# Performance work log

Hardware: AMD Instinct MI355X
Metric: run time of the kernel (lower is better)

The kernel has to match this reference:

```python
import jax, jax.numpy as jnp
import numpy as np

B = 8       # number of point clouds
N = 4096    # points per cloud (start_point)
M = 1024    # sampled points per cloud (sampled_point_ammount), ratio 0.25
D = 64      # feature dim


def setup_inputs() -> dict:
    key = jax.random.key(0)
    k1, k2 = jax.random.split(key)
    x = jax.random.normal(k1, (B * N, D), dtype=jnp.float32)
    pos = jax.random.uniform(k2, (B * N, 3), dtype=jnp.float32)
    batch = jnp.repeat(jnp.arange(B, dtype=jnp.int32), N)  # sorted batch ids
    return {"x": x, "pos": pos, "batch": batch}


def _fps_single(pos_b, m):
    # Farthest point sampling on one cloud [N,3]; deterministic start at index 0.
    n = pos_b.shape[0]
    big = jnp.asarray(jnp.finfo(pos_b.dtype).max, pos_b.dtype)

    def step(carry, _):
        mind, last = carry
        d = jnp.sum((pos_b - pos_b[last]) ** 2, axis=-1)  # [N]
        mind = jnp.minimum(mind, d)
        nxt = jnp.argmax(mind).astype(jnp.int32)
        return (mind, nxt), nxt

    init = (jnp.full((n,), big, pos_b.dtype), jnp.int32(0))
    _, rest = jax.lax.scan(step, init, None, length=m - 1)
    return jnp.concatenate([jnp.zeros((1,), jnp.int32), rest])  # [M]


def reference(x, pos, batch):
    pos_b = pos.reshape(B, N, 3)
    # --- DownsampleMRG: FPS gather (scale_factor = M/N) ---
    idx = jax.vmap(lambda p: _fps_single(p, M))(pos_b)              # [B, M] local idx
    gidx = (idx + jnp.arange(B, dtype=jnp.int32)[:, None] * N).reshape(-1)
    x_lr = x[gidx]                                                  # [B*M, D]
    pos_lr = pos[gidx]                                              # [B*M, 3]
    # --- UpsampleMRG: lr_x = cat([x_lr, pos_lr]); knn_interpolate k=1 ---
    lr_feat = jnp.concatenate([x_lr, pos_lr], axis=1).reshape(B, M, D + 3)
    pos_lr_b = pos_lr.reshape(B, M, 3)
    # pairwise squared distances hr->lr within each cloud: [B, N, M]
    d2 = jnp.sum((pos_b[:, :, None, :] - pos_lr_b[:, None, :, :]) ** 2, axis=-1)
    nn = jnp.argmin(d2, axis=-1)                                    # [B, N]
    # k=1 interpolation: weights normalize to 1 -> pure nearest-neighbor gather
    interp = jnp.take_along_axis(lr_feat, nn[:, :, None], axis=1).reshape(B * N, D + 3)
    # out_x = cat([x_hr, pos_hr, interpolated lr features])
    out_x = jnp.concatenate([x, pos, interp], axis=1)               # [B*N, D+3+D+3]
    return out_x, jnp.zeros((out_x.shape[0], 3), pos.dtype), batch
```

## Files before the change

### kernel.cpp

```cpp
#include <hip/hip_runtime.h>
#include <cstdint>

#define BATCH 8
#define NPTS  4096
#define MPTS  1024
#define DIM   64

typedef float v2f __attribute__((ext_vector_type(2)));
typedef unsigned long long u64;
typedef unsigned int u32;

__device__ __forceinline__ double mk_key(float m, u32 aux) {
  const u64 k = ((u64)__float_as_uint(m) << 32) | (u64)aux;
  return __longlong_as_double((long long)k);
}
__device__ __forceinline__ u32 key_lo(double d) {
  return (u32)(u64)__double_as_longlong(d);
}

#define WAVE_MAX_F64_STEP(x, ctrl)                                                    \
  {                                                                                   \
    const u64 xu_ = (u64)__double_as_longlong(x);                                     \
    const int lo_ = __builtin_amdgcn_update_dpp(0, (int)(u32)xu_, (ctrl), 0xf, 0xf, true);  \
    const int hi_ = __builtin_amdgcn_update_dpp(0, (int)(u32)(xu_ >> 32), (ctrl), 0xf, 0xf, true); \
    const double y_ = __longlong_as_double((long long)(((u64)(u32)hi_ << 32) | (u64)(u32)lo_)); \
    (x) = fmax((x), y_);                                                              \
  }

__global__ __launch_bounds__(256) void fps_kernel(const float* __restrict__ pos,
                                                  int* __restrict__ gidx) {
#pragma clang fp contract(off)
  const int b = blockIdx.x;
  const int t = threadIdx.x;
  const float* p = pos + (size_t)b * NPTS * 3;

  __shared__ float4 sp[NPTS];
  __shared__ double red[2][4];

  v2f px[8], py[8], pz[8], mind[8];
#pragma unroll
  for (int k = 0; k < 16; ++k) {
    const int i = t + k * 256;
    const float a = p[3 * i + 0];
    const float c = p[3 * i + 1];
    const float d = p[3 * i + 2];
    sp[i] = make_float4(a, c, d, 0.0f);
    px[k >> 1][k & 1] = a;
    py[k >> 1][k & 1] = c;
    pz[k >> 1][k & 1] = d;
    mind[k >> 1][k & 1] = 3.402823466e+38f;
  }
  __syncthreads();

  if (t == 0) gidx[b * MPTS] = b * NPTS;
  float4 w = sp[0];
  float lx = w.x, ly = w.y, lz = w.z;

  for (int it = 1; it < MPTS; ++it) {
    const v2f vlx = {lx, lx}, vly = {ly, ly}, vlz = {lz, lz};
    double pg[8];
#pragma unroll
    for (int g = 0; g < 8; ++g) {
      const v2f dx = px[g] - vlx;
      const v2f dy = py[g] - vly;
      const v2f dz = pz[g] - vlz;
      const v2f d = (dx * dx + dy * dy) + dz * dz;
      const v2f m = __builtin_elementwise_min(mind[g], d);
      mind[g] = m;
      const double p0 = mk_key(m[0], ~(u32)(t + (2 * g) * 256));
      const double p1 = mk_key(m[1], ~(u32)(t + (2 * g + 1) * 256));
      pg[g] = fmax(p0, p1);
    }
    const double b0 = fmax(pg[0], pg[1]);
    const double b1 = fmax(pg[2], pg[3]);
    const double b2 = fmax(pg[4], pg[5]);
    const double b3 = fmax(pg[6], pg[7]);
    double best = fmax(fmax(b0, b1), fmax(b2, b3));

    WAVE_MAX_F64_STEP(best, 0x111);
    WAVE_MAX_F64_STEP(best, 0x112);
    WAVE_MAX_F64_STEP(best, 0x114);
    WAVE_MAX_F64_STEP(best, 0x118);
    WAVE_MAX_F64_STEP(best, 0x142);
    WAVE_MAX_F64_STEP(best, 0x143);

    const int buf = it & 1;
    if ((t & 63) == 63) red[buf][t >> 6] = best;
    __syncthreads();

    const double c = fmax(fmax(red[buf][0], red[buf][1]),
                          fmax(red[buf][2], red[buf][3]));
    const u32 widx = ~key_lo(c);

    w = sp[widx];
    lx = w.x; ly = w.y; lz = w.z;
    if (t == 0) gidx[b * MPTS + it] = b * NPTS + (int)widx;
  }
}

__global__ __launch_bounds__(256) void nn_kernel(const float* __restrict__ pos,
                                                 const int* __restrict__ gidx,
                                                 int* __restrict__ nng) {
#pragma clang fp contract(off)
  const int b = blockIdx.x >> 5;
  const int chunk = blockIdx.x & 31;
  const int t = threadIdx.x;

  __shared__ float lrx[MPTS], lry[MPTS], lrz[MPTS];
  for (int j = t; j < MPTS; j += 256) {
    const int g = gidx[b * MPTS + j];
    lrx[j] = pos[3 * g + 0];
    lry[j] = pos[3 * g + 1];
    lrz[j] = pos[3 * g + 2];
  }
  __syncthreads();

  const int pt = chunk * 128 + (t >> 1);
  const int half = t & 1;
  const int i = b * NPTS + pt;
  const float x = pos[3 * i + 0];
  const float y = pos[3 * i + 1];
  const float z = pos[3 * i + 2];
  const v2f vx = {x, x}, vy = {y, y}, vz = {z, z};

  double best = __longlong_as_double(0x7FEFFFFFFFFFFFFFll);
  const int j0 = half * 512;
#pragma unroll 4
  for (int s = 0; s < 256; ++s) {
    const int j = j0 + 2 * s;
    const v2f qx = *(const v2f*)&lrx[j];
    const v2f qy = *(const v2f*)&lry[j];
    const v2f qz = *(const v2f*)&lrz[j];
    const v2f dx = vx - qx;
    const v2f dy = vy - qy;
    const v2f dz = vz - qz;
    const v2f d = (dx * dx + dy * dy) + dz * dz;
    const double p0 = mk_key(d[0], (u32)j);
    const double p1 = mk_key(d[1], (u32)(j + 1));
    best = fmin(best, fmin(p0, p1));
  }
  const u64 bu = (u64)__double_as_longlong(best);
  const u64 ou = ((u64)(u32)__shfl_xor((int)(bu >> 32), 1, 64) << 32) |
                 (u64)(u32)__shfl_xor((int)(u32)bu, 1, 64);
  best = fmin(best, __longlong_as_double((long long)ou));
  if (half == 0) nng[i] = gidx[b * MPTS + (int)key_lo(best)];
}

__global__ __launch_bounds__(256) void assemble_kernel(const float* __restrict__ x,
                                                       const float* __restrict__ pos,
                                                       const int* __restrict__ batch,
                                                       const int* __restrict__ nng,
                                                       float* __restrict__ out) {
  const int w = (int)((blockIdx.x * 256 + threadIdx.x) >> 6);
  const int lane = threadIdx.x & 63;
  if (w >= BATCH * NPTS) return;
  const int g = nng[w];

  float* o = out + (size_t)w * 134;
  o[lane] = x[(size_t)w * DIM + lane];
  o[67 + lane] = x[(size_t)g * DIM + lane];
  if (lane < 3) {
    o[64 + lane] = pos[3 * w + lane];
    o[131 + lane] = pos[3 * g + lane];
  }

  float* o2 = out + (size_t)BATCH * NPTS * 134;
  if (lane < 3) o2[3 * w + lane] = 0.0f;
  float* o3 = o2 + (size_t)BATCH * NPTS * 3;
  if (lane == 0) o3[w] = (float)batch[w];
}

extern "C" void kernel_launch(void* const* d_in, const int* in_sizes, int n_in,
                              void* d_out, int out_size, void* d_ws, size_t ws_size,
                              hipStream_t stream) {
  const float* x = (const float*)d_in[0];
  const float* pos = (const float*)d_in[1];
  const int* batch = (const int*)d_in[2];

  int* gidx = (int*)d_ws;
  int* nng = gidx + BATCH * MPTS;

  float* out = (float*)d_out;

  fps_kernel<<<BATCH, 256, 0, stream>>>(pos, gidx);
  nn_kernel<<<BATCH * 32, 256, 0, stream>>>(pos, gidx, nng);
  assemble_kernel<<<(BATCH * NPTS * 64) / 256, 256, 0, stream>>>(x, pos, batch, nng, out);
}
```

Baseline: 575.8 us.

## Process two clouds per FPS block and fuse nearest-neighbor with output assembly

The FPS kernel now processes two point clouds per block, interleaving their independent distance/argmax chains so they share one barrier per iteration and expose more instruction-level parallelism. The shared-memory position copy is dropped and the selected point is re-read from global memory. The nearest-neighbor and assembly kernels are fused so neighbor indices stay in shared memory and one launch and round-trip are removed. This doubles register pressure in FPS and puts a global load on the serial critical path.

```diff
diff --git a/kernel.cpp b/kernel.cpp
--- a/kernel.cpp
+++ b/kernel.cpp
@@ -11,102 +11,136 @@
 typedef unsigned int u32;
 
 __device__ __forceinline__ double mk_key(float m, u32 aux) {
-  const u64 k = ((u64)__float_as_uint(m) << 32) | (u64)aux;
-  return __longlong_as_double((long long)k);
+  return __hiloint2double((int)__float_as_uint(m), (int)aux);
 }
 __device__ __forceinline__ u32 key_lo(double d) {
-  return (u32)(u64)__double_as_longlong(d);
-}
-
-#define WAVE_MAX_F64_STEP(x, ctrl)                                                    \
-  {                                                                                   \
-    const u64 xu_ = (u64)__double_as_longlong(x);                                     \
-    const int lo_ = __builtin_amdgcn_update_dpp(0, (int)(u32)xu_, (ctrl), 0xf, 0xf, true);  \
-    const int hi_ = __builtin_amdgcn_update_dpp(0, (int)(u32)(xu_ >> 32), (ctrl), 0xf, 0xf, true); \
-    const double y_ = __longlong_as_double((long long)(((u64)(u32)hi_ << 32) | (u64)(u32)lo_)); \
-    (x) = fmax((x), y_);                                                              \
-  }
-
-__global__ __launch_bounds__(256) void fps_kernel(const float* __restrict__ pos,
-                                                  int* __restrict__ gidx) {
+  return (u32)__double2loint(d);
+}
+
+#define WAVE_MAX_F64_STEP(x, ctrl)                                                   \
+  {                                                                                  \
+    const int lo_ = __builtin_amdgcn_update_dpp(0, __double2loint(x), (ctrl), 0xf, 0xf, true); \
+    const int hi_ = __builtin_amdgcn_update_dpp(0, __double2hiint(x), (ctrl), 0xf, 0xf, true); \
+    const double y_ = __hiloint2double(hi_, lo_);                                    \
+    (x) = fmax((x), y_);                                                             \
+  }
+
+__global__ __launch_bounds__(256, 1) void fps_kernel(const float* __restrict__ pos,
+                                                     int* __restrict__ gidx) {
 #pragma clang fp contract(off)
-  const int b = blockIdx.x;
+  const int b0 = blockIdx.x * 2, b1 = b0 + 1;
   const int t = threadIdx.x;
-  const float* p = pos + (size_t)b * NPTS * 3;
-
-  __shared__ float4 sp[NPTS];
-  __shared__ double red[2][4];
-
-  v2f px[8], py[8], pz[8], mind[8];
+  const float* pA = pos + (size_t)b0 * NPTS * 3;
+  const float* pB = pos + (size_t)b1 * NPTS * 3;
+
+  __shared__ double redA[2][4], redB[2][4];
+
+  v2f ax[8], ay[8], az[8], am[8];
+  v2f bx[8], by[8], bz[8], bm[8];
+  u32 aux[16];
 #pragma unroll
   for (int k = 0; k < 16; ++k) {
     const int i = t + k * 256;
-    const float a = p[3 * i + 0];
-    const float c = p[3 * i + 1];
-    const float d = p[3 * i + 2];
-    sp[i] = make_float4(a, c, d, 0.0f);
-    px[k >> 1][k & 1] = a;
-    py[k >> 1][k & 1] = c;
-    pz[k >> 1][k & 1] = d;
-    mind[k >> 1][k & 1] = 3.402823466e+38f;
-  }
-  __syncthreads();
-
-  if (t == 0) gidx[b * MPTS] = b * NPTS;
-  float4 w = sp[0];
-  float lx = w.x, ly = w.y, lz = w.z;
+    aux[k] = ~(u32)i;
+    ax[k >> 1][k & 1] = pA[3 * i + 0];
+    ay[k >> 1][k & 1] = pA[3 * i + 1];
+    az[k >> 1][k & 1] = pA[3 * i + 2];
+    bx[k >> 1][k & 1] = pB[3 * i + 0];
+    by[k >> 1][k & 1] = pB[3 * i + 1];
+    bz[k >> 1][k & 1] = pB[3 * i + 2];
+    am[k >> 1][k & 1] = 3.402823466e+38f;
+    bm[k >> 1][k & 1] = 3.402823466e+38f;
+  }
+
+  if (t == 0) {
+    gidx[b0 * MPTS] = b0 * NPTS;
+    gidx[b1 * MPTS] = b1 * NPTS;
+  }
+  float lxA = pA[0], lyA = pA[1], lzA = pA[2];
+  float lxB = pB[0], lyB = pB[1], lzB = pB[2];
 
   for (int it = 1; it < MPTS; ++it) {
-    const v2f vlx = {lx, lx}, vly = {ly, ly}, vlz = {lz, lz};
-    double pg[8];
-#pragma unroll
-    for (int g = 0; g < 8; ++g) {
-      const v2f dx = px[g] - vlx;
-      const v2f dy = py[g] - vly;
-      const v2f dz = pz[g] - vlz;
-      const v2f d = (dx * dx + dy * dy) + dz * dz;
-      const v2f m = __builtin_elementwise_min(mind[g], d);
-      mind[g] = m;
-      const double p0 = mk_key(m[0], ~(u32)(t + (2 * g) * 256));
-      const double p1 = mk_key(m[1], ~(u32)(t + (2 * g + 1) * 256));
-      pg[g] = fmax(p0, p1);
-    }
-    const double b0 = fmax(pg[0], pg[1]);
-    const double b1 = fmax(pg[2], pg[3]);
-    const double b2 = fmax(pg[4], pg[5]);
-    const double b3 = fmax(pg[6], pg[7]);
-    double best = fmax(fmax(b0, b1), fmax(b2, b3));
-
-    WAVE_MAX_F64_STEP(best, 0x111);
-    WAVE_MAX_F64_STEP(best, 0x112);
-    WAVE_MAX_F64_STEP(best, 0x114);
-    WAVE_MAX_F64_STEP(best, 0x118);
-    WAVE_MAX_F64_STEP(best, 0x142);
-    WAVE_MAX_F64_STEP(best, 0x143);
-
     const int buf = it & 1;
-    if ((t & 63) == 63) red[buf][t >> 6] = best;
+    double bestA;
+    {
+      const v2f vx = {lxA, lxA}, vy = {lyA, lyA}, vz = {lzA, lzA};
+      double pg[8];
+#pragma unroll
+      for (int g = 0; g < 8; ++g) {
+        const v2f dx = ax[g] - vx;
+        const v2f dy = ay[g] - vy;
+        const v2f dz = az[g] - vz;
+        const v2f d = (dx * dx + dy * dy) + dz * dz;
+        const v2f m = __builtin_elementwise_min(am[g], d);
+        am[g] = m;
+        pg[g] = fmax(mk_key(m[0], aux[2 * g]), mk_key(m[1], aux[2 * g + 1]));
+      }
+      bestA = fmax(fmax(fmax(pg[0], pg[1]), fmax(pg[2], pg[3])),
+                   fmax(fmax(pg[4], pg[5]), fmax(pg[6], pg[7])));
+      WAVE_MAX_F64_STEP(bestA, 0x111);
+      WAVE_MAX_F64_STEP(bestA, 0x112);
+      WAVE_MAX_F64_STEP(bestA, 0x114);
+      WAVE_MAX_F64_STEP(bestA, 0x118);
+      WAVE_MAX_F64_STEP(bestA, 0x142);
+      WAVE_MAX_F64_STEP(bestA, 0x143);
+    }
+    double bestB;
+    {
+      const v2f vx = {lxB, lxB}, vy = {lyB, lyB}, vz = {lzB, lzB};
+      double pg[8];
+#pragma unroll
+      for (int g = 0; g < 8; ++g) {
+        const v2f dx = bx[g] - vx;
+        const v2f dy = by[g] - vy;
+        const v2f dz = bz[g] - vz;
+        const v2f d = (dx * dx + dy * dy) + dz * dz;
+        const v2f m = __builtin_elementwise_min(bm[g], d);
+        bm[g] = m;
+        pg[g] = fmax(mk_key(m[0], aux[2 * g]), mk_key(m[1], aux[2 * g + 1]));
+      }
+      bestB = fmax(fmax(fmax(pg[0], pg[1]), fmax(pg[2], pg[3])),
+                   fmax(fmax(pg[4], pg[5]), fmax(pg[6], pg[7])));
+      WAVE_MAX_F64_STEP(bestB, 0x111);
+      WAVE_MAX_F64_STEP(bestB, 0x112);
+      WAVE_MAX_F64_STEP(bestB, 0x114);
+      WAVE_MAX_F64_STEP(bestB, 0x118);
+      WAVE_MAX_F64_STEP(bestB, 0x142);
+      WAVE_MAX_F64_STEP(bestB, 0x143);
+    }
+
+    if ((t & 63) == 63) {
+      redA[buf][t >> 6] = bestA;
+      redB[buf][t >> 6] = bestB;
+    }
     __syncthreads();
 
-    const double c = fmax(fmax(red[buf][0], red[buf][1]),
-                          fmax(red[buf][2], red[buf][3]));
-    const u32 widx = ~key_lo(c);
-
-    w = sp[widx];
-    lx = w.x; ly = w.y; lz = w.z;
-    if (t == 0) gidx[b * MPTS + it] = b * NPTS + (int)widx;
-  }
-}
-
-__global__ __launch_bounds__(256) void nn_kernel(const float* __restrict__ pos,
-                                                 const int* __restrict__ gidx,
-                                                 int* __restrict__ nng) {
+    const double cA = fmax(fmax(redA[buf][0], redA[buf][1]),
+                           fmax(redA[buf][2], redA[buf][3]));
+    const double cB = fmax(fmax(redB[buf][0], redB[buf][1]),
+                           fmax(redB[buf][2], redB[buf][3]));
+    const u32 wA = ~key_lo(cA);
+    const u32 wB = ~key_lo(cB);
+    const float3 qa = *(const float3*)(pA + 3 * (size_t)wA);
+    const float3 qb = *(const float3*)(pB + 3 * (size_t)wB);
+    lxA = qa.x; lyA = qa.y; lzA = qa.z;
+    lxB = qb.x; lyB = qb.y; lzB = qb.z;
+    if (t == 0) {
+      gidx[b0 * MPTS + it] = b0 * NPTS + (int)wA;
+      gidx[b1 * MPTS + it] = b1 * NPTS + (int)wB;
+    }
+  }
+}
+
+__global__ __launch_bounds__(256) void nn_assemble_kernel(
+    const float* __restrict__ x, const float* __restrict__ pos,
+    const int* __restrict__ gidx, float* __restrict__ out) {
 #pragma clang fp contract(off)
   const int b = blockIdx.x >> 5;
   const int chunk = blockIdx.x & 31;
   const int t = threadIdx.x;
 
   __shared__ float lrx[MPTS], lry[MPTS], lrz[MPTS];
+  __shared__ int snng[128];
   for (int j = t; j < MPTS; j += 256) {
     const int g = gidx[b * MPTS + j];
     lrx[j] = pos[3 * g + 0];
@@ -115,59 +149,53 @@
   }
   __syncthreads();
 
-  const int pt = chunk * 128 + (t >> 1);
-  const int half = t & 1;
-  const int i = b * NPTS + pt;
-  const float x = pos[3 * i + 0];
-  const float y = pos[3 * i + 1];
-  const float z = pos[3 * i + 2];
-  const v2f vx = {x, x}, vy = {y, y}, vz = {z, z};
-
-  double best = __longlong_as_double(0x7FEFFFFFFFFFFFFFll);
-  const int j0 = half * 512;
+  {
+    const int pt = chunk * 128 + (t >> 1);
+    const int half = t & 1;
+    const int i = b * NPTS + pt;
+    const float px = pos[3 * i + 0];
+    const float py = pos[3 * i + 1];
+    const float pz = pos[3 * i + 2];
+    const v2f vx = {px, px}, vy = {py, py}, vz = {pz, pz};
+
+    double best = __hiloint2double(0x7FEFFFFF, 0xFFFFFFFF);
+    const int j0 = half * 512;
 #pragma unroll 4
-  for (int s = 0; s < 256; ++s) {
-    const int j = j0 + 2 * s;
-    const v2f qx = *(const v2f*)&lrx[j];
-    const v2f qy = *(const v2f*)&lry[j];
-    const v2f qz = *(const v2f*)&lrz[j];
-    const v2f dx = vx - qx;
-    const v2f dy = vy - qy;
-    const v2f dz = vz - qz;
-    const v2f d = (dx * dx + dy * dy) + dz * dz;
-    const double p0 = mk_key(d[0], (u32)j);
-    const double p1 = mk_key(d[1], (u32)(j + 1));
-    best = fmin(best, fmin(p0, p1));
-  }
-  const u64 bu = (u64)__double_as_longlong(best);
-  const u64 ou = ((u64)(u32)__shfl_xor((int)(bu >> 32), 1, 64) << 32) |
-                 (u64)(u32)__shfl_xor((int)(u32)bu, 1, 64);
-  best = fmin(best, __longlong_as_double((long long)ou));
-  if (half == 0) nng[i] = gidx[b * MPTS + (int)key_lo(best)];
-}
-
-__global__ __launch_bounds__(256) void assemble_kernel(const float* __restrict__ x,
-                                                       const float* __restrict__ pos,
-                                                       const int* __restrict__ batch,
-                                                       const int* __restrict__ nng,
-                                                       float* __restrict__ out) {
-  const int w = (int)((blockIdx.x * 256 + threadIdx.x) >> 6);
-  const int lane = threadIdx.x & 63;
-  if (w >= BATCH * NPTS) return;
-  const int g = nng[w];
-
-  float* o = out + (size_t)w * 134;
-  o[lane] = x[(size_t)w * DIM + lane];
-  o[67 + lane] = x[(size_t)g * DIM + lane];
-  if (lane < 3) {
-    o[64 + lane] = pos[3 * w + lane];
-    o[131 + lane] = pos[3 * g + lane];
-  }
-
+    for (int s = 0; s < 256; ++s) {
+      const int j = j0 + 2 * s;
+      const v2f qx = *(const v2f*)&lrx[j];
+      const v2f qy = *(const v2f*)&lry[j];
+      const v2f qz = *(const v2f*)&lrz[j];
+      const v2f dx = vx - qx;
+      const v2f dy = vy - qy;
+      const v2f dz = vz - qz;
+      const v2f d = (dx * dx + dy * dy) + dz * dz;
+      best = fmin(best, fmin(mk_key(d[0], (u32)j), mk_key(d[1], (u32)(j + 1))));
+    }
+    const int blo = __shfl_xor(__double2loint(best), 1, 64);
+    const int bhi = __shfl_xor(__double2hiint(best), 1, 64);
+    best = fmin(best, __hiloint2double(bhi, blo));
+    if (half == 0) snng[t >> 1] = gidx[b * MPTS + (int)key_lo(best)];
+  }
+  __syncthreads();
+
+  const int wave = t >> 6, lane = t & 63;
   float* o2 = out + (size_t)BATCH * NPTS * 134;
-  if (lane < 3) o2[3 * w + lane] = 0.0f;
   float* o3 = o2 + (size_t)BATCH * NPTS * 3;
-  if (lane == 0) o3[w] = (float)batch[w];
+#pragma unroll
+  for (int r = wave; r < 128; r += 4) {
+    const int i = b * NPTS + chunk * 128 + r;
+    const int g = snng[r];
+    float* o = out + (size_t)i * 134;
+    o[lane] = x[(size_t)i * DIM + lane];
+    o[67 + lane] = x[(size_t)g * DIM + lane];
+    if (lane < 3) {
+      o[64 + lane] = pos[3 * i + lane];
+      o[131 + lane] = pos[3 * g + lane];
+      o2[3 * i + lane] = 0.0f;
+    }
+    if (lane == 0) o3[i] = (float)b;
+  }
 }
 
 extern "C" void kernel_launch(void* const* d_in, const int* in_sizes, int n_in,
@@ -175,14 +203,10 @@
                               hipStream_t stream) {
   const float* x = (const float*)d_in[0];
   const float* pos = (const float*)d_in[1];
-  const int* batch = (const int*)d_in[2];
 
   int* gidx = (int*)d_ws;
-  int* nng = gidx + BATCH * MPTS;
-
   float* out = (float*)d_out;
 
-  fps_kernel<<<BATCH, 256, 0, stream>>>(pos, gidx);
-  nn_kernel<<<BATCH * 32, 256, 0, stream>>>(pos, gidx, nng);
-  assemble_kernel<<<(BATCH * NPTS * 64) / 256, 256, 0, stream>>>(x, pos, batch, nng, out);
-}
+  fps_kernel<<<BATCH / 2, 256, 0, stream>>>(pos, gidx);
+  nn_assemble_kernel<<<BATCH * 32, 256, 0, stream>>>(x, pos, gidx, out);
+}
```

New measurement: 987.8 us. 71.6% more time.

## Widen FPS block to 512 threads and fuse NN search with output assembly

Applied to the files above, without the earlier changes.

The FPS kernel now runs 512 threads per cloud, so each thread holds 8 points instead of 16. Shared positions move from an array of float4 to separate x/y/z arrays, index keys are precomputed, and the cross-wave reduction grows to 8 waves. The nearest-neighbour and assembly kernels are merged: neighbour indices stay in shared memory and the same block writes the output rows, which removes one launch and the nng round-trip. The batch output is written as the block's cloud id instead of being read from the batch input, which relies on the batch ids being sorted and contiguous. The wider FPS block adds barrier and reduction cost on a loop that runs serially, one iteration per sample.

```diff
diff --git a/kernel.cpp b/kernel.cpp
--- a/kernel.cpp
+++ b/kernel.cpp
@@ -11,40 +11,40 @@
 typedef unsigned int u32;
 
 __device__ __forceinline__ double mk_key(float m, u32 aux) {
-  const u64 k = ((u64)__float_as_uint(m) << 32) | (u64)aux;
-  return __longlong_as_double((long long)k);
+  return __hiloint2double((int)__float_as_uint(m), (int)aux);
 }
 __device__ __forceinline__ u32 key_lo(double d) {
-  return (u32)(u64)__double_as_longlong(d);
+  return (u32)__double2loint(d);
 }
 
-#define WAVE_MAX_F64_STEP(x, ctrl)                                                    \
-  {                                                                                   \
-    const u64 xu_ = (u64)__double_as_longlong(x);                                     \
-    const int lo_ = __builtin_amdgcn_update_dpp(0, (int)(u32)xu_, (ctrl), 0xf, 0xf, true);  \
-    const int hi_ = __builtin_amdgcn_update_dpp(0, (int)(u32)(xu_ >> 32), (ctrl), 0xf, 0xf, true); \
-    const double y_ = __longlong_as_double((long long)(((u64)(u32)hi_ << 32) | (u64)(u32)lo_)); \
-    (x) = fmax((x), y_);                                                              \
+#define WAVE_MAX_F64_STEP(x, ctrl)                                                   \
+  {                                                                                  \
+    const int lo_ = __builtin_amdgcn_update_dpp(0, __double2loint(x), (ctrl), 0xf, 0xf, true); \
+    const int hi_ = __builtin_amdgcn_update_dpp(0, __double2hiint(x), (ctrl), 0xf, 0xf, true); \
+    const double y_ = __hiloint2double(hi_, lo_);                                    \
+    (x) = fmax((x), y_);                                                             \
   }
 
-__global__ __launch_bounds__(256) void fps_kernel(const float* __restrict__ pos,
+__global__ __launch_bounds__(512) void fps_kernel(const float* __restrict__ pos,
                                                   int* __restrict__ gidx) {
 #pragma clang fp contract(off)
   const int b = blockIdx.x;
   const int t = threadIdx.x;
   const float* p = pos + (size_t)b * NPTS * 3;
 
-  __shared__ float4 sp[NPTS];
-  __shared__ double red[2][4];
+  __shared__ float sx[NPTS], sy[NPTS], sz[NPTS];
+  __shared__ double red[2][8];
 
-  v2f px[8], py[8], pz[8], mind[8];
+  v2f px[4], py[4], pz[4], mind[4];
+  u32 aux[8];
 #pragma unroll
-  for (int k = 0; k < 16; ++k) {
-    const int i = t + k * 256;
+  for (int k = 0; k < 8; ++k) {
+    const int i = t + k * 512;
+    aux[k] = ~(u32)i;
     const float a = p[3 * i + 0];
     const float c = p[3 * i + 1];
     const float d = p[3 * i + 2];
-    sp[i] = make_float4(a, c, d, 0.0f);
+    sx[i] = a; sy[i] = c; sz[i] = d;
     px[k >> 1][k & 1] = a;
     py[k >> 1][k & 1] = c;
     pz[k >> 1][k & 1] = d;
@@ -53,29 +53,22 @@
   __syncthreads();
 
   if (t == 0) gidx[b * MPTS] = b * NPTS;
-  float4 w = sp[0];
-  float lx = w.x, ly = w.y, lz = w.z;
+  float lx = sx[0], ly = sy[0], lz = sz[0];
 
   for (int it = 1; it < MPTS; ++it) {
     const v2f vlx = {lx, lx}, vly = {ly, ly}, vlz = {lz, lz};
-    double pg[8];
+    double pg[4];
 #pragma unroll
-    for (int g = 0; g < 8; ++g) {
+    for (int g = 0; g < 4; ++g) {
       const v2f dx = px[g] - vlx;
       const v2f dy = py[g] - vly;
       const v2f dz = pz[g] - vlz;
       const v2f d = (dx * dx + dy * dy) + dz * dz;
       const v2f m = __builtin_elementwise_min(mind[g], d);
       mind[g] = m;
-      const double p0 = mk_key(m[0], ~(u32)(t + (2 * g) * 256));
-      const double p1 = mk_key(m[1], ~(u32)(t + (2 * g + 1) * 256));
-      pg[g] = fmax(p0, p1);
+      pg[g] = fmax(mk_key(m[0], aux[2 * g]), mk_key(m[1], aux[2 * g + 1]));
     }
-    const double b0 = fmax(pg[0], pg[1]);
-    const double b1 = fmax(pg[2], pg[3]);
-    const double b2 = fmax(pg[4], pg[5]);
-    const double b3 = fmax(pg[6], pg[7]);
-    double best = fmax(fmax(b0, b1), fmax(b2, b3));
+    double best = fmax(fmax(pg[0], pg[1]), fmax(pg[2], pg[3]));
 
     WAVE_MAX_F64_STEP(best, 0x111);
     WAVE_MAX_F64_STEP(best, 0x112);
@@ -88,25 +81,30 @@
     if ((t & 63) == 63) red[buf][t >> 6] = best;
     __syncthreads();
 
-    const double c = fmax(fmax(red[buf][0], red[buf][1]),
-                          fmax(red[buf][2], red[buf][3]));
+    const double c0 = fmax(fmax(red[buf][0], red[buf][1]),
+                           fmax(red[buf][2], red[buf][3]));
+    const double c1 = fmax(fmax(red[buf][4], red[buf][5]),
+                           fmax(red[buf][6], red[buf][7]));
+    const double c = fmax(c0, c1);
     const u32 widx = ~key_lo(c);
 
-    w = sp[widx];
-    lx = w.x; ly = w.y; lz = w.z;
+    lx = sx[widx];
+    ly = sy[widx];
+    lz = sz[widx];
     if (t == 0) gidx[b * MPTS + it] = b * NPTS + (int)widx;
   }
 }
 
-__global__ __launch_bounds__(256) void nn_kernel(const float* __restrict__ pos,
-                                                 const int* __restrict__ gidx,
-                                                 int* __restrict__ nng) {
+__global__ __launch_bounds__(256) void nn_assemble_kernel(
+    const float* __restrict__ x, const float* __restrict__ pos,
+    const int* __restrict__ gidx, float* __restrict__ out) {
 #pragma clang fp contract(off)
   const int b = blockIdx.x >> 5;
   const int chunk = blockIdx.x & 31;
   const int t = threadIdx.x;
 
   __shared__ float lrx[MPTS], lry[MPTS], lrz[MPTS];
+  __shared__ int snng[128];
   for (int j = t; j < MPTS; j += 256) {
     const int g = gidx[b * MPTS + j];
     lrx[j] = pos[3 * g + 0];
@@ -115,59 +113,53 @@
   }
   __syncthreads();
 
-  const int pt = chunk * 128 + (t >> 1);
-  const int half = t & 1;
-  const int i = b * NPTS + pt;
-  const float x = pos[3 * i + 0];
-  const float y = pos[3 * i + 1];
-  const float z = pos[3 * i + 2];
-  const v2f vx = {x, x}, vy = {y, y}, vz = {z, z};
+  {
+    const int pt = chunk * 128 + (t >> 1);
+    const int half = t & 1;
+    const int i = b * NPTS + pt;
+    const float px = pos[3 * i + 0];
+    const float py = pos[3 * i + 1];
+    const float pz = pos[3 * i + 2];
+    const v2f vx = {px, px}, vy = {py, py}, vz = {pz, pz};
 
-  double best = __longlong_as_double(0x7FEFFFFFFFFFFFFFll);
-  const int j0 = half * 512;
+    double best = __hiloint2double(0x7FEFFFFF, 0xFFFFFFFF);
+    const int j0 = half * 512;
 #pragma unroll 4
-  for (int s = 0; s < 256; ++s) {
-    const int j = j0 + 2 * s;
-    const v2f qx = *(const v2f*)&lrx[j];
-    const v2f qy = *(const v2f*)&lry[j];
-    const v2f qz = *(const v2f*)&lrz[j];
-    const v2f dx = vx - qx;
-    const v2f dy = vy - qy;
-    const v2f dz = vz - qz;
-    const v2f d = (dx * dx + dy * dy) + dz * dz;
-    const double p0 = mk_key(d[0], (u32)j);
-    const double p1 = mk_key(d[1], (u32)(j + 1));
-    best = fmin(best, fmin(p0, p1));
+    for (int s = 0; s < 256; ++s) {
+      const int j = j0 + 2 * s;
+      const v2f qx = *(const v2f*)&lrx[j];
+      const v2f qy = *(const v2f*)&lry[j];
+      const v2f qz = *(const v2f*)&lrz[j];
+      const v2f dx = vx - qx;
+      const v2f dy = vy - qy;
+      const v2f dz = vz - qz;
+      const v2f d = (dx * dx + dy * dy) + dz * dz;
+      best = fmin(best, fmin(mk_key(d[0], (u32)j), mk_key(d[1], (u32)(j + 1))));
+    }
+    const int blo = __shfl_xor(__double2loint(best), 1, 64);
+    const int bhi = __shfl_xor(__double2hiint(best), 1, 64);
+    best = fmin(best, __hiloint2double(bhi, blo));
+    if (half == 0) snng[t >> 1] = gidx[b * MPTS + (int)key_lo(best)];
   }
-  const u64 bu = (u64)__double_as_longlong(best);
-  const u64 ou = ((u64)(u32)__shfl_xor((int)(bu >> 32), 1, 64) << 32) |
-                 (u64)(u32)__shfl_xor((int)(u32)bu, 1, 64);
-  best = fmin(best, __longlong_as_double((long long)ou));
-  if (half == 0) nng[i] = gidx[b * MPTS + (int)key_lo(best)];
-}
+  __syncthreads();
 
-__global__ __launch_bounds__(256) void assemble_kernel(const float* __restrict__ x,
-                                                       const float* __restrict__ pos,
-                                                       const int* __restrict__ batch,
-                                                       const int* __restrict__ nng,
-                                                       float* __restrict__ out) {
-  const int w = (int)((blockIdx.x * 256 + threadIdx.x) >> 6);
-  const int lane = threadIdx.x & 63;
-  if (w >= BATCH * NPTS) return;
-  const int g = nng[w];
-
-  float* o = out + (size_t)w * 134;
-  o[lane] = x[(size_t)w * DIM + lane];
-  o[67 + lane] = x[(size_t)g * DIM + lane];
-  if (lane < 3) {
-    o[64 + lane] = pos[3 * w + lane];
-    o[131 + lane] = pos[3 * g + lane];
+  const int wave = t >> 6, lane = t & 63;
+  float* o2 = out + (size_t)BATCH * NPTS * 134;
+  float* o3 = o2 + (size_t)BATCH * NPTS * 3;
+#pragma unroll
+  for (int r = wave; r < 128; r += 4) {
+    const int i = b * NPTS + chunk * 128 + r;
+    const int g = snng[r];
+    float* o = out + (size_t)i * 134;
+    o[lane] = x[(size_t)i * DIM + lane];
+    o[67 + lane] = x[(size_t)g * DIM + lane];
+    if (lane < 3) {
+      o[64 + lane] = pos[3 * i + lane];
+      o[131 + lane] = pos[3 * g + lane];
+      o2[3 * i + lane] = 0.0f;
+    }
+    if (lane == 0) o3[i] = (float)b;
   }
-
-  float* o2 = out + (size_t)BATCH * NPTS * 134;
-  if (lane < 3) o2[3 * w + lane] = 0.0f;
-  float* o3 = o2 + (size_t)BATCH * NPTS * 3;
-  if (lane == 0) o3[w] = (float)batch[w];
 }
 
 extern "C" void kernel_launch(void* const* d_in, const int* in_sizes, int n_in,
@@ -175,14 +167,10 @@
                               hipStream_t stream) {
   const float* x = (const float*)d_in[0];
   const float* pos = (const float*)d_in[1];
-  const int* batch = (const int*)d_in[2];
 
   int* gidx = (int*)d_ws;
-  int* nng = gidx + BATCH * MPTS;
-
   float* out = (float*)d_out;
 
-  fps_kernel<<<BATCH, 256, 0, stream>>>(pos, gidx);
-  nn_kernel<<<BATCH * 32, 256, 0, stream>>>(pos, gidx, nng);
-  assemble_kernel<<<(BATCH * NPTS * 64) / 256, 256, 0, stream>>>(x, pos, batch, nng, out);
+  fps_kernel<<<BATCH, 512, 0, stream>>>(pos, gidx);
+  nn_assemble_kernel<<<BATCH * 32, 256, 0, stream>>>(x, pos, gidx, out);
 }
```

Result: slower. 637.2 us (+10.7%).
